# Performance work log

Measured on AMD Instinct MI355X. Metric: run time of the kernel, lower is better.

Reference implementation:

```python
import jax, jax.numpy as jnp
import numpy as np

N_NODES = 40000
N_EDGES = 640000
D = 128
BN_EPS = 1e-5
LEAKY_SLOPE = 0.01


def setup_inputs() -> dict:
    key = jax.random.key(0)
    k1, k2, k3, k4, k5 = jax.random.split(key, 5)
    node_feat = jax.random.normal(k1, (N_NODES, D), dtype=jnp.float32)
    edge_feat = jax.random.normal(k2, (N_EDGES, D), dtype=jnp.float32)
    edge_src = jax.random.randint(k3, (N_EDGES,), 0, N_NODES, dtype=jnp.int32)
    edge_dst = jax.random.randint(k4, (N_EDGES,), 0, N_NODES, dtype=jnp.int32)
    W = jax.random.normal(k5, (D, D), dtype=jnp.float32) * (1.0 / np.sqrt(D))
    b = jnp.zeros((D,), dtype=jnp.float32)
    gamma = jnp.ones((D,), dtype=jnp.float32)
    beta = jnp.zeros((D,), dtype=jnp.float32)
    return {"node_feat": node_feat, "edge_feat": edge_feat,
            "edge_src": edge_src, "edge_dst": edge_dst,
            "W": W, "b": b, "gamma": gamma, "beta": beta}


def reference(node_feat, edge_feat, edge_src, edge_dst, W, b, gamma, beta):
    # message: m = relu(h_src + h_e), per edge  [E, D]
    m = jax.nn.relu(node_feat[edge_src] + edge_feat)
    # reduce: sum messages into destination nodes  [N, D]
    neigh = jax.ops.segment_sum(m, edge_dst, num_segments=node_feat.shape[0])
    # residual then MLP: Linear -> (Dropout=identity in eval) -> LeakyReLU -> BatchNorm1d
    rst = node_feat + neigh
    y = rst @ W.T + b
    y = jnp.where(y >= 0, y, LEAKY_SLOPE * y)
    mean = jnp.mean(y, axis=0)
    var = jnp.mean((y - mean) ** 2, axis=0)  # biased variance, as torch BN uses
    y = (y - mean) * jax.lax.rsqrt(var + BN_EPS) * gamma + beta
    return y
```

## Files before the change

kernel.cpp:

```cpp
#include <hip/hip_runtime.h>

constexpr int NN = 40000;
constexpr int NE = 640000;
constexpr int DD = 128;
constexpr int TN = 128;
constexpr int SCAN_B = 40;
constexpr size_t WS_STATS = 0;
constexpr size_t WS_BSUM  = 2048;
constexpr size_t WS_CNT   = 4096;
constexpr size_t WS_OFFS  = 167936;
constexpr size_t WS_CURS  = 335872;
constexpr size_t WS_PAIRS = 499712;
constexpr size_t WS_NEEDED = WS_PAIRS + (size_t)NE * 8;

__global__ __launch_bounds__(256) void k_zero(int* __restrict__ cnt,
                                              float* __restrict__ stats) {
    int i = blockIdx.x * 256 + threadIdx.x;
    if (i < SCAN_B * 1024) cnt[i] = 0;
    else if (i < SCAN_B * 1024 + 512) stats[i - SCAN_B * 1024] = 0.0f;
}

__global__ __launch_bounds__(256) void k_hist(const int* __restrict__ edst,
                                              int* __restrict__ cnt) {
    int e = blockIdx.x * 256 + threadIdx.x;
    if (e < NE) atomicAdd(&cnt[edst[e]], 1);
}

__global__ void k_scanA(const int* __restrict__ cnt, int* __restrict__ bsum) {
    __shared__ int sm[1024];
    int tid = threadIdx.x;
    sm[tid] = cnt[blockIdx.x * 1024 + tid];
    __syncthreads();
    for (int s = 512; s > 0; s >>= 1) {
        if (tid < s) sm[tid] += sm[tid + s];
        __syncthreads();
    }
    if (tid == 0) bsum[blockIdx.x] = sm[0];
}

__global__ void k_scanB(int* __restrict__ bsum) {
    if (threadIdx.x == 0) {
        int run = 0;
        for (int b = 0; b < SCAN_B; ++b) { int t = bsum[b]; bsum[b] = run; run += t; }
    }
}

__global__ void k_scanC(const int* __restrict__ cnt, const int* __restrict__ bsum,
                        int* __restrict__ offs, int* __restrict__ curs) {
    __shared__ int sm[1024];
    int tid = threadIdx.x;
    int i = blockIdx.x * 1024 + tid;
    int v = cnt[i];
    sm[tid] = v;
    __syncthreads();
    for (int off = 1; off < 1024; off <<= 1) {
        int add = (tid >= off) ? sm[tid - off] : 0;
        __syncthreads();
        sm[tid] += add;
        __syncthreads();
    }
    int excl = sm[tid] - v + bsum[blockIdx.x];
    offs[i] = excl;
    if (i < NN) curs[i] = excl;
}

__global__ __launch_bounds__(256) void k_scatter(const int* __restrict__ esrc,
                                                 const int* __restrict__ edst,
                                                 int* __restrict__ curs,
                                                 int2* __restrict__ pairs) {
    int e = blockIdx.x * 256 + threadIdx.x;
    if (e < NE) {
        int d = edst[e];
        int pos = atomicAdd(&curs[d], 1);
        pairs[pos] = make_int2(esrc[e], e);
    }
}

__global__ __launch_bounds__(256) void k_gather(const float* __restrict__ nf,
                                                const float* __restrict__ ef,
                                                const int* __restrict__ offs,
                                                const int2* __restrict__ pairs,
                                                float* __restrict__ y) {
    int gt = blockIdx.x * 256 + threadIdx.x;
    int n = gt >> 6;
    int lane = threadIdx.x & 63;
    const float2* ef2 = (const float2*)ef;
    const float2* nf2 = (const float2*)nf;
    int start = offs[n];
    int end   = offs[n + 1];
    float2 acc = nf2[(size_t)n * 64 + lane];
    for (int base = start; base < end; base += 64) {
        int idx = base + lane;
        int2 pr = (idx < end) ? pairs[idx] : make_int2(0, 0);
        int cnt = min(64, end - base);
        for (int i = 0; i < cnt; ++i) {
            int s = __shfl(pr.x, i);
            int e = __shfl(pr.y, i);
            float2 a = ef2[(size_t)e * 64 + lane];
            float2 b = nf2[(size_t)s * 64 + lane];
            acc.x += fmaxf(a.x + b.x, 0.0f);
            acc.y += fmaxf(a.y + b.y, 0.0f);
        }
    }
    reinterpret_cast<float2*>(y)[(size_t)n * 64 + lane] = acc;
}

__global__ __launch_bounds__(256) void k_init(const float* __restrict__ nf,
                                              float* __restrict__ acc,
                                              float* __restrict__ stats) {
    int i = blockIdx.x * 256 + threadIdx.x;
    reinterpret_cast<float4*>(acc)[i] = reinterpret_cast<const float4*>(nf)[i];
    if (blockIdx.x == 0) stats[threadIdx.x] = 0.0f;
}

__global__ __launch_bounds__(256) void k_edge(const float* __restrict__ nf,
                                              const float* __restrict__ ef,
                                              const int* __restrict__ esrc,
                                              const int* __restrict__ edst,
                                              float* __restrict__ acc) {
    const unsigned total = (unsigned)NE * 32u;
    const unsigned stride = gridDim.x * 256u;
    for (unsigned gid = blockIdx.x * 256u + threadIdx.x; gid < total; gid += stride) {
        unsigned e = gid >> 5;
        unsigned c = gid & 31u;
        int s = esrc[e];
        int d = edst[e];
        float4 hs = reinterpret_cast<const float4*>(nf + (size_t)s * DD)[c];
        float4 he = reinterpret_cast<const float4*>(ef + (size_t)e * DD)[c];
        float4 m;
        m.x = fmaxf(hs.x + he.x, 0.0f);
        m.y = fmaxf(hs.y + he.y, 0.0f);
        m.z = fmaxf(hs.z + he.z, 0.0f);
        m.w = fmaxf(hs.w + he.w, 0.0f);
        float* p = acc + (size_t)d * DD + c * 4u;
        unsafeAtomicAdd(p + 0, m.x);
        unsafeAtomicAdd(p + 1, m.y);
        unsafeAtomicAdd(p + 2, m.z);
        unsafeAtomicAdd(p + 3, m.w);
    }
}

__global__ __launch_bounds__(256, 1) void k_mlp(float* __restrict__ y,
                                                const float* __restrict__ Wm,
                                                const float* __restrict__ bias,
                                                float* __restrict__ stats) {
    __shared__ float Ws[DD][DD];
    __shared__ float As[TN][DD];
    __shared__ float ssum[DD];
    __shared__ float ssumsq[DD];

    const int tid = threadIdx.x;
    const int n0 = blockIdx.x * TN;

    for (int i = tid; i < DD * (DD / 4); i += 256) {
        int j  = i >> 5;
        int k4 = i & 31;
        float4 w = reinterpret_cast<const float4*>(Wm + j * DD)[k4];
        int ks = (k4 * 4) ^ (((j >> 4) & 7) << 2);
        *reinterpret_cast<float4*>(&Ws[j][ks]) = w;
    }
    for (int i = tid; i < TN * (DD / 4); i += 256) {
        int nl = i >> 5;
        int k4 = i & 31;
        int n  = n0 + nl;
        float4 a = make_float4(0.f, 0.f, 0.f, 0.f);
        if (n < NN) a = reinterpret_cast<const float4*>(y + (size_t)n * DD)[k4];
        int ks = (k4 * 4) ^ (((nl >> 2) & 7) << 2);
        *reinterpret_cast<float4*>(&As[nl][ks]) = a;
    }
    if (tid < DD) { ssum[tid] = 0.0f; ssumsq[tid] = 0.0f; }
    __syncthreads();

    const int ng = tid >> 3;
    const int jg = tid & 7;
    const int aswz = (ng & 7) << 2;
    const int wswz = jg << 2;
    const int nb = 4 * ng;

    float acc4[4][16];
#pragma unroll
    for (int i = 0; i < 4; ++i)
#pragma unroll
        for (int jj = 0; jj < 16; ++jj) acc4[i][jj] = 0.0f;

#pragma unroll 2
    for (int t = 0; t < DD / 4; ++t) {
        const int ka = (4 * t) ^ aswz;
        const int kw = (4 * t) ^ wswz;
        float4 a0 = *reinterpret_cast<const float4*>(&As[nb + 0][ka]);
        float4 a1 = *reinterpret_cast<const float4*>(&As[nb + 1][ka]);
        float4 a2 = *reinterpret_cast<const float4*>(&As[nb + 2][ka]);
        float4 a3 = *reinterpret_cast<const float4*>(&As[nb + 3][ka]);
#pragma unroll
        for (int jj = 0; jj < 16; ++jj) {
            float4 w = *reinterpret_cast<const float4*>(&Ws[16 * jg + jj][kw]);
            acc4[0][jj] = fmaf(a0.x, w.x, fmaf(a0.y, w.y, fmaf(a0.z, w.z, fmaf(a0.w, w.w, acc4[0][jj]))));
            acc4[1][jj] = fmaf(a1.x, w.x, fmaf(a1.y, w.y, fmaf(a1.z, w.z, fmaf(a1.w, w.w, acc4[1][jj]))));
            acc4[2][jj] = fmaf(a2.x, w.x, fmaf(a2.y, w.y, fmaf(a2.z, w.z, fmaf(a2.w, w.w, acc4[2][jj]))));
            acc4[3][jj] = fmaf(a3.x, w.x, fmaf(a3.y, w.y, fmaf(a3.z, w.z, fmaf(a3.w, w.w, acc4[3][jj]))));
        }
    }

    float psum[16], psq[16];
#pragma unroll
    for (int jj = 0; jj < 16; ++jj) { psum[jj] = 0.0f; psq[jj] = 0.0f; }

#pragma unroll
    for (int i = 0; i < 4; ++i) {
        int n = n0 + nb + i;
        if (n < NN) {
            float out[16];
#pragma unroll
            for (int jj = 0; jj < 16; ++jj) {
                float v = acc4[i][jj] + bias[16 * jg + jj];
                v = (v >= 0.0f) ? v : 0.01f * v;
                out[jj] = v;
                psum[jj] += v;
                psq[jj]  += v * v;
            }
            float4* dst = reinterpret_cast<float4*>(y + (size_t)n * DD + 16 * jg);
            dst[0] = make_float4(out[0],  out[1],  out[2],  out[3]);
            dst[1] = make_float4(out[4],  out[5],  out[6],  out[7]);
            dst[2] = make_float4(out[8],  out[9],  out[10], out[11]);
            dst[3] = make_float4(out[12], out[13], out[14], out[15]);
        }
    }
#pragma unroll
    for (int jj = 0; jj < 16; ++jj) {
        atomicAdd(&ssum[16 * jg + jj], psum[jj]);
        atomicAdd(&ssumsq[16 * jg + jj], psq[jj]);
    }
    __syncthreads();
    if (tid < DD) {
        unsafeAtomicAdd(&stats[tid],      ssum[tid]);
        unsafeAtomicAdd(&stats[DD + tid], ssumsq[tid]);
    }
}

__global__ void k_stats(float* __restrict__ stats,
                        const float* __restrict__ gamma,
                        const float* __restrict__ beta) {
    int j = threadIdx.x;
    if (j < DD) {
        float inv_n = 1.0f / (float)NN;
        float mean = stats[j] * inv_n;
        float var  = stats[DD + j] * inv_n - mean * mean;
        float s = gamma[j] * rsqrtf(var + 1e-5f);
        stats[2 * DD + j] = s;
        stats[3 * DD + j] = beta[j] - mean * s;
    }
}

__global__ __launch_bounds__(256) void k_bn(float* __restrict__ y,
                                            const float* __restrict__ stats) {
    int i = blockIdx.x * 256 + threadIdx.x;
    int k4 = i & 31;
    float4 sc = reinterpret_cast<const float4*>(stats + 2 * DD)[k4];
    float4 sh = reinterpret_cast<const float4*>(stats + 3 * DD)[k4];
    float4 v = reinterpret_cast<float4*>(y)[i];
    v.x = fmaf(v.x, sc.x, sh.x);
    v.y = fmaf(v.y, sc.y, sh.y);
    v.z = fmaf(v.z, sc.z, sh.z);
    v.w = fmaf(v.w, sc.w, sh.w);
    reinterpret_cast<float4*>(y)[i] = v;
}

extern "C" void kernel_launch(void* const* d_in, const int* in_sizes, int n_in,
                              void* d_out, int out_size, void* d_ws, size_t ws_size,
                              hipStream_t stream) {
    const float* nf    = (const float*)d_in[0];
    const float* ef    = (const float*)d_in[1];
    const int*   esrc  = (const int*)d_in[2];
    const int*   edst  = (const int*)d_in[3];
    const float* Wm    = (const float*)d_in[4];
    const float* bias  = (const float*)d_in[5];
    const float* gamma = (const float*)d_in[6];
    const float* beta  = (const float*)d_in[7];
    float* y = (float*)d_out;
    char* ws = (char*)d_ws;

    float* stats = (float*)(ws + WS_STATS);
    int*   bsum  = (int*)(ws + WS_BSUM);
    int*   cnt   = (int*)(ws + WS_CNT);
    int*   offs  = (int*)(ws + WS_OFFS);
    int*   curs  = (int*)(ws + WS_CURS);
    int2*  pairs = (int2*)(ws + WS_PAIRS);

    const int vec_blocks = (NN * DD / 4) / 256;
    const int edge_blocks = (NE + 255) / 256;

    if (ws_size >= WS_NEEDED) {
        k_zero<<<(SCAN_B * 1024 + 512 + 255) / 256, 256, 0, stream>>>(cnt, stats);
        k_hist<<<edge_blocks, 256, 0, stream>>>(edst, cnt);
        k_scanA<<<SCAN_B, 1024, 0, stream>>>(cnt, bsum);
        k_scanB<<<1, 64, 0, stream>>>(bsum);
        k_scanC<<<SCAN_B, 1024, 0, stream>>>(cnt, bsum, offs, curs);
        k_scatter<<<edge_blocks, 256, 0, stream>>>(esrc, edst, curs, pairs);
        k_gather<<<NN * 64 / 256, 256, 0, stream>>>(nf, ef, offs, pairs, y);
    } else {
        k_init<<<vec_blocks, 256, 0, stream>>>(nf, y, stats);
        k_edge<<<2048, 256, 0, stream>>>(nf, ef, esrc, edst, y);
    }
    k_mlp<<<(NN + TN - 1) / TN, 256, 0, stream>>>(y, Wm, bias, stats);
    k_stats<<<1, 128, 0, stream>>>(stats, gamma, beta);
    k_bn<<<vec_blocks, 256, 0, stream>>>(y, stats);
}
```

Before: 643.8 us.

## Single-block scan and float4 half-wave edge gather

```diff
diff --git a/kernel.cpp b/kernel.cpp
--- a/kernel.cpp
+++ b/kernel.cpp
@@ -4,9 +4,10 @@
 constexpr int NE = 640000;
 constexpr int DD = 128;
 constexpr int TN = 128;
-constexpr int SCAN_B = 40;
+constexpr int SCAN_N = 40960;
+constexpr int SCAN_T = 1024;
+constexpr int SCAN_PER = SCAN_N / SCAN_T;
 constexpr size_t WS_STATS = 0;
-constexpr size_t WS_BSUM  = 2048;
 constexpr size_t WS_CNT   = 4096;
 constexpr size_t WS_OFFS  = 167936;
 constexpr size_t WS_CURS  = 335872;
@@ -16,8 +17,8 @@
 __global__ __launch_bounds__(256) void k_zero(int* __restrict__ cnt,
                                               float* __restrict__ stats) {
     int i = blockIdx.x * 256 + threadIdx.x;
-    if (i < SCAN_B * 1024) cnt[i] = 0;
-    else if (i < SCAN_B * 1024 + 512) stats[i - SCAN_B * 1024] = 0.0f;
+    if (i < SCAN_N) cnt[i] = 0;
+    else if (i < SCAN_N + 512) stats[i - SCAN_N] = 0.0f;
 }
 
 __global__ __launch_bounds__(256) void k_hist(const int* __restrict__ edst,
@@ -26,42 +27,32 @@
     if (e < NE) atomicAdd(&cnt[edst[e]], 1);
 }
 
-__global__ void k_scanA(const int* __restrict__ cnt, int* __restrict__ bsum) {
-    __shared__ int sm[1024];
-    int tid = threadIdx.x;
-    sm[tid] = cnt[blockIdx.x * 1024 + tid];
+__global__ __launch_bounds__(1024) void k_scan(const int* __restrict__ cnt,
+                                               int* __restrict__ offs,
+                                               int* __restrict__ curs) {
+    __shared__ int sm[SCAN_T];
+    int t = threadIdx.x;
+    int base = t * SCAN_PER;
+    int run = 0;
+#pragma unroll
+    for (int i = 0; i < SCAN_PER; ++i) run += cnt[base + i];
+    sm[t] = run;
     __syncthreads();
-    for (int s = 512; s > 0; s >>= 1) {
-        if (tid < s) sm[tid] += sm[tid + s];
+    for (int off = 1; off < SCAN_T; off <<= 1) {
+        int add = (t >= off) ? sm[t - off] : 0;
         __syncthreads();
-    }
-    if (tid == 0) bsum[blockIdx.x] = sm[0];
-}
-
-__global__ void k_scanB(int* __restrict__ bsum) {
-    if (threadIdx.x == 0) {
-        int run = 0;
-        for (int b = 0; b < SCAN_B; ++b) { int t = bsum[b]; bsum[b] = run; run += t; }
-    }
-}
-
-__global__ void k_scanC(const int* __restrict__ cnt, const int* __restrict__ bsum,
-                        int* __restrict__ offs, int* __restrict__ curs) {
-    __shared__ int sm[1024];
-    int tid = threadIdx.x;
-    int i = blockIdx.x * 1024 + tid;
-    int v = cnt[i];
-    sm[tid] = v;
-    __syncthreads();
-    for (int off = 1; off < 1024; off <<= 1) {
-        int add = (tid >= off) ? sm[tid - off] : 0;
+        sm[t] += add;
         __syncthreads();
-        sm[tid] += add;
-        __syncthreads();
-    }
-    int excl = sm[tid] - v + bsum[blockIdx.x];
-    offs[i] = excl;
-    if (i < NN) curs[i] = excl;
+    }
+    int excl = sm[t] - run;
+#pragma unroll
+    for (int i = 0; i < SCAN_PER; ++i) {
+        int v = cnt[base + i];
+        offs[base + i] = excl;
+        if (base + i < NN) curs[base + i] = excl;
+        excl += v;
+    }
+    if (t == SCAN_T - 1) offs[SCAN_N] = excl;
 }
 
 __global__ __launch_bounds__(256) void k_scatter(const int* __restrict__ esrc,
@@ -84,25 +75,42 @@
     int gt = blockIdx.x * 256 + threadIdx.x;
     int n = gt >> 6;
     int lane = threadIdx.x & 63;
-    const float2* ef2 = (const float2*)ef;
-    const float2* nf2 = (const float2*)nf;
+    int h  = lane >> 5;
+    int il = lane & 31;
+    const float4* ef4 = (const float4*)ef;
+    const float4* nf4 = (const float4*)nf;
     int start = offs[n];
     int end   = offs[n + 1];
-    float2 acc = nf2[(size_t)n * 64 + lane];
+    float4 acc = make_float4(0.f, 0.f, 0.f, 0.f);
     for (int base = start; base < end; base += 64) {
         int idx = base + lane;
         int2 pr = (idx < end) ? pairs[idx] : make_int2(0, 0);
         int cnt = min(64, end - base);
-        for (int i = 0; i < cnt; ++i) {
-            int s = __shfl(pr.x, i);
-            int e = __shfl(pr.y, i);
-            float2 a = ef2[(size_t)e * 64 + lane];
-            float2 b = nf2[(size_t)s * 64 + lane];
-            acc.x += fmaxf(a.x + b.x, 0.0f);
-            acc.y += fmaxf(a.y + b.y, 0.0f);
+        int nit = (cnt + 1) >> 1;
+        for (int i = 0; i < nit; ++i) {
+            int j = 2 * i + h;
+            int s = __shfl(pr.x, j);
+            int e = __shfl(pr.y, j);
+            if (j < cnt) {
+                float4 a = ef4[(size_t)e * 32 + il];
+                float4 b = nf4[(size_t)s * 32 + il];
+                acc.x += fmaxf(a.x + b.x, 0.0f);
+                acc.y += fmaxf(a.y + b.y, 0.0f);
+                acc.z += fmaxf(a.z + b.z, 0.0f);
+                acc.w += fmaxf(a.w + b.w, 0.0f);
+            }
         }
     }
-    reinterpret_cast<float2*>(y)[(size_t)n * 64 + lane] = acc;
+    float4 r;
+    r.x = acc.x + __shfl_xor(acc.x, 32);
+    r.y = acc.y + __shfl_xor(acc.y, 32);
+    r.z = acc.z + __shfl_xor(acc.z, 32);
+    r.w = acc.w + __shfl_xor(acc.w, 32);
+    if (h == 0) {
+        float4 b = nf4[(size_t)n * 32 + il];
+        r.x += b.x; r.y += b.y; r.z += b.z; r.w += b.w;
+        reinterpret_cast<float4*>(y)[(size_t)n * 32 + il] = r;
+    }
 }
 
 __global__ __launch_bounds__(256) void k_init(const float* __restrict__ nf,
@@ -280,7 +288,6 @@
     char* ws = (char*)d_ws;
 
     float* stats = (float*)(ws + WS_STATS);
-    int*   bsum  = (int*)(ws + WS_BSUM);
     int*   cnt   = (int*)(ws + WS_CNT);
     int*   offs  = (int*)(ws + WS_OFFS);
     int*   curs  = (int*)(ws + WS_CURS);
@@ -290,11 +297,9 @@
     const int edge_blocks = (NE + 255) / 256;
 
     if (ws_size >= WS_NEEDED) {
-        k_zero<<<(SCAN_B * 1024 + 512 + 255) / 256, 256, 0, stream>>>(cnt, stats);
+        k_zero<<<(SCAN_N + 512 + 255) / 256, 256, 0, stream>>>(cnt, stats);
         k_hist<<<edge_blocks, 256, 0, stream>>>(edst, cnt);
-        k_scanA<<<SCAN_B, 1024, 0, stream>>>(cnt, bsum);
-        k_scanB<<<1, 64, 0, stream>>>(bsum);
-        k_scanC<<<SCAN_B, 1024, 0, stream>>>(cnt, bsum, offs, curs);
+        k_scan<<<1, SCAN_T, 0, stream>>>(cnt, offs, curs);
         k_scatter<<<edge_blocks, 256, 0, stream>>>(esrc, edst, curs, pairs);
         k_gather<<<NN * 64 / 256, 256, 0, stream>>>(nf, ef, offs, pairs, y);
     } else {
```

New measurement: 684.6 us. 6.3% more time.
